# Kernel optimization log

Measured on AMD Instinct MI355X. Metric: run time of the kernel, lower is better.

The kernel has to match this reference:

```python
import jax, jax.numpy as jnp
import numpy as np

D_MODEL, D_INNER, D_STATE, DT_RANK, K = 768, 1536, 16, 48, 4
B, L = 2, 1024


def causal_depthwise_conv(x, w, b):
    # x: [B, L, D], w: [D, 1, K], b: [D]; torch pads K-1 both sides then slices [:L] -> causal left pad
    xt = x.transpose(0, 2, 1)  # [B, D, L]
    out = jax.lax.conv_general_dilated(
        xt, w, window_strides=(1,), padding=[(K - 1, 0)],
        dimension_numbers=('NCH', 'OIH', 'NCH'), feature_group_count=xt.shape[1])
    return out.transpose(0, 2, 1) + b


def ssm(xc, A_log, D, W_dt, dtW, dtb, W_B, W_C):
    # xc: [B, L, Din]
    A = -jnp.exp(A_log)                                   # [Din, N]
    dt_low = jnp.einsum('bld,rd->blr', xc, W_dt)          # [B, L, R]
    delta = jax.nn.softplus(jnp.einsum('blr,dr->bld', dt_low, dtW) + dtb)  # [B, L, Din]
    Bm = jnp.einsum('bld,nd->bln', xc, W_B)               # [B, L, N]
    Cm = jnp.einsum('bld,nd->bln', xc, W_C)               # [B, L, N]
    deltaA = jnp.exp(delta[..., None] * A)                # [B, L, Din, N]
    BX = (delta * xc)[..., None] * Bm[:, :, None, :]      # [B, L, Din, N]

    def combine(e1, e2):
        a1, b1 = e1
        a2, b2 = e2
        return a1 * a2, a2 * b1 + b2

    _, hs = jax.lax.associative_scan(combine, (deltaA, BX), axis=1)  # [B, L, Din, N]
    y = jnp.einsum('bldn,bln->bld', hs, Cm) + D * xc
    return y


def setup_inputs() -> dict:
    key = jax.random.key(0)
    ks = jax.random.split(key, 20)
    s = 0.02
    A_init = jnp.log(jnp.broadcast_to(jnp.arange(1, D_STATE + 1, dtype=jnp.float32), (D_INNER, D_STATE)))
    return {
        'x': jax.random.normal(ks[0], (B, L, D_MODEL), jnp.float32),
        'W_in_states': jax.random.normal(ks[1], (D_INNER, D_MODEL), jnp.float32) * s,
        'W_in_gates': jax.random.normal(ks[2], (D_INNER, D_MODEL), jnp.float32) * s,
        'conv_w': jax.random.normal(ks[3], (D_INNER, 1, K), jnp.float32) * 0.2,
        'conv_b': jax.random.normal(ks[4], (D_INNER,), jnp.float32) * 0.02,
        'conv_w_b': jax.random.normal(ks[5], (D_INNER, 1, K), jnp.float32) * 0.2,
        'conv_b_b': jax.random.normal(ks[6], (D_INNER,), jnp.float32) * 0.02,
        'W_dt': jax.random.normal(ks[7], (DT_RANK, D_INNER), jnp.float32) * s,
        'W_B': jax.random.normal(ks[8], (D_STATE, D_INNER), jnp.float32) * s,
        'W_C': jax.random.normal(ks[9], (D_STATE, D_INNER), jnp.float32) * s,
        'dtW': jax.random.normal(ks[10], (D_INNER, DT_RANK), jnp.float32) * s,
        'dtb': jax.random.normal(ks[11], (D_INNER,), jnp.float32) * 0.1,
        'A_log': A_init,
        'Dp': jnp.ones((D_INNER,), jnp.float32),
        'W_dt_b': jax.random.normal(ks[12], (DT_RANK, D_INNER), jnp.float32) * s,
        'W_B_b': jax.random.normal(ks[13], (D_STATE, D_INNER), jnp.float32) * s,
        'W_C_b': jax.random.normal(ks[14], (D_STATE, D_INNER), jnp.float32) * s,
        'dtW_b': jax.random.normal(ks[15], (D_INNER, DT_RANK), jnp.float32) * s,
        'dtb_b': jax.random.normal(ks[16], (D_INNER,), jnp.float32) * 0.1,
        'A_log_b': A_init,
        'Dp_b': jnp.ones((D_INNER,), jnp.float32),
        'W_out': jax.random.normal(ks[17], (D_MODEL, D_INNER), jnp.float32) * s,
    }


def reference(x, W_in_states, W_in_gates, conv_w, conv_b, conv_w_b, conv_b_b,
              W_dt, W_B, W_C, dtW, dtb, A_log, Dp,
              W_dt_b, W_B_b, W_C_b, dtW_b, dtb_b, A_log_b, Dp_b, W_out):
    xs = jnp.einsum('blm,dm->bld', x, W_in_states)  # [B, L, Din]
    z = jnp.einsum('blm,dm->bld', x, W_in_gates)    # [B, L, Din]
    # forward branch
    xc = jax.nn.silu(causal_depthwise_conv(xs, conv_w, conv_b))
    y = ssm(xc, A_log, Dp, W_dt, dtW, dtb, W_B, W_C)
    # backward branch: xz flipped along L, split -> reversed xs / reversed z
    xs_b = xs[:, ::-1]
    z_b = z[:, ::-1]
    xcb = jax.nn.silu(causal_depthwise_conv(xs_b, conv_w_b, conv_b_b))
    y_b = ssm(xcb, A_log_b, Dp_b, W_dt_b, dtW_b, dtb_b, W_B_b, W_C_b)
    # gating
    y = y * jax.nn.silu(z)
    y_b = y_b * jax.nn.silu(z_b)
    y = (y + y_b[:, ::-1]) * 0.5  # divide_output
    return jnp.einsum('bld,md->blm', y, W_out)
```

## Files before the change

### kernel.cpp

```cpp
#include <hip/hip_runtime.h>
#include <hip/hip_bf16.h>
#include <stdint.h>

#define DM 768
#define DI 1536
#define DSTATE 16
#define RNK 48
#define BB 2
#define LL 1024
#define ML (BB * LL)

#define NSEG 32
#define SEGL (LL / NSEG)

typedef unsigned short u16;
typedef __bf16 bf16x8 __attribute__((ext_vector_type(8)));
typedef float f32x4 __attribute__((ext_vector_type(4)));

struct __align__(8) u16x4_t { u16 x, y, z, w; };

__device__ __forceinline__ float b2f(u16 u) {
  union { uint32_t i; float f; } v; v.i = ((uint32_t)u) << 16; return v.f;
}
__device__ __forceinline__ u16 f2b(float f) {
  union { float f; uint32_t i; } v; v.f = f;
  uint32_t r = v.i + 0x7FFFu + ((v.i >> 16) & 1u);
  return (u16)(r >> 16);
}
__device__ __forceinline__ float silu_f(float x) { return x / (1.f + __expf(-x)); }
__device__ __forceinline__ float softplus_f(float s) {
  return fmaxf(s, 0.f) + __logf(1.f + __expf(-fabsf(s)));
}
__device__ __forceinline__ u16x4_t cvt4(float4 v) {
  u16x4_t o; o.x = f2b(v.x); o.y = f2b(v.y); o.z = f2b(v.z); o.w = f2b(v.w); return o;
}

#define SEG_X    (ML * DM / 4)
#define SEG_W    (DI * DM / 4)
#define SEG_CAT  (128 * DI / 4)
#define SEG_DTW  (DI * 64 / 4)
__global__ __launch_bounds__(256) void convert_kernel(
    const float4* __restrict__ x, const float4* __restrict__ wis,
    const float4* __restrict__ wig, const float4* __restrict__ wout,
    const float* __restrict__ W_B, const float* __restrict__ W_C,
    const float* __restrict__ W_dt,
    const float* __restrict__ W_B_b, const float* __restrict__ W_C_b,
    const float* __restrict__ W_dt_b,
    const float* __restrict__ dtW, const float* __restrict__ dtW_b,
    u16x4_t* __restrict__ xb, u16x4_t* __restrict__ wisb,
    u16x4_t* __restrict__ wigb, u16x4_t* __restrict__ woutb,
    u16x4_t* __restrict__ wcf, u16x4_t* __restrict__ wcb,
    u16x4_t* __restrict__ dtwf, u16x4_t* __restrict__ dtwb)
{
  int idx = blockIdx.x * 256 + threadIdx.x;
  if (idx < SEG_X) { xb[idx] = cvt4(x[idx]); return; }
  idx -= SEG_X;
  if (idx < SEG_W) { wisb[idx] = cvt4(wis[idx]); return; }
  idx -= SEG_W;
  if (idx < SEG_W) { wigb[idx] = cvt4(wig[idx]); return; }
  idx -= SEG_W;
  if (idx < SEG_W) { woutb[idx] = cvt4(wout[idx]); return; }
  idx -= SEG_W;
  if (idx < 2 * SEG_CAT) {
    int dir = idx / SEG_CAT;
    int rem = idx % SEG_CAT;
    int row = rem / (DI / 4), k4 = rem % (DI / 4);
    const float* src = nullptr;
    if (row < 16)      src = (dir ? W_B_b  : W_B)  + (size_t)row * DI + k4 * 4;
    else if (row < 32) src = (dir ? W_C_b  : W_C)  + (size_t)(row - 16) * DI + k4 * 4;
    else if (row < 80) src = (dir ? W_dt_b : W_dt) + (size_t)(row - 32) * DI + k4 * 4;
    u16x4_t o;
    if (src) o = cvt4(*(const float4*)src);
    else { o.x = 0; o.y = 0; o.z = 0; o.w = 0; }
    (dir ? wcb : wcf)[rem] = o;
    return;
  }
  idx -= 2 * SEG_CAT;
  int dir = idx / SEG_DTW;
  int rem = idx % SEG_DTW;
  int d = rem / 16, r4 = rem % 16;
  const float* Dw = dir ? dtW_b : dtW;
  u16x4_t o;
  if (r4 < 12) o = cvt4(*(const float4*)(Dw + (size_t)d * RNK + r4 * 4));
  else { o.x = 0; o.y = 0; o.z = 0; o.w = 0; }
  (dir ? dtwb : dtwf)[rem] = o;
}

__global__ __launch_bounds__(256) void gemm_bt(
    const u16* __restrict__ A, const u16* __restrict__ B0,
    const u16* __restrict__ B1, int Nsplit,
    void* __restrict__ Cout, int M, int N, int K, int ldc, int epi,
    const u16* __restrict__ A2, const u16* __restrict__ B2,
    void* __restrict__ C2,
    u16* __restrict__ Caux, u16* __restrict__ Caux2,
    const float* __restrict__ ebias, const float* __restrict__ ebias2)
{
  if (blockIdx.z) { A = A2; B0 = B2; Cout = C2; Caux = Caux2; ebias = ebias2; }
  __shared__ alignas(16) u16 As[128 * 32];
  __shared__ alignas(16) u16 Bs[128 * 32];
  const int tid = threadIdx.x;
  const int wave = tid >> 6, lane = tid & 63;
  const int bm = blockIdx.y * 128;
  const int bn = blockIdx.x * 128;

  const u16* Bmat = B0;
  int ncol0 = bn;
  int epi_l = epi;
  if (B1 != nullptr && bn >= Nsplit) { Bmat = B1; ncol0 = bn - Nsplit; epi_l = 1; }

  const int c0 = tid, c1 = tid + 256;
  const u16* gA0 = A + (size_t)(bm + (c0 >> 2)) * K + (c0 & 3) * 8;
  const u16* gA1 = A + (size_t)(bm + (c1 >> 2)) * K + (c1 & 3) * 8;
  const u16* gB0 = Bmat + (size_t)(ncol0 + (c0 >> 2)) * K + (c0 & 3) * 8;
  const u16* gB1 = Bmat + (size_t)(ncol0 + (c1 >> 2)) * K + (c1 & 3) * 8;
  uint4* lA0 = (uint4*)&As[c0 * 8]; uint4* lA1 = (uint4*)&As[c1 * 8];
  uint4* lB0 = (uint4*)&Bs[c0 * 8]; uint4* lB1 = (uint4*)&Bs[c1 * 8];

  const int wm = (wave & 1) * 64, wn = (wave >> 1) * 64;
  const int rl = lane & 15, q = lane >> 4;

  f32x4 acc[4][4];
#pragma unroll
  for (int i = 0; i < 4; ++i)
#pragma unroll
    for (int j = 0; j < 4; ++j) acc[i][j] = (f32x4){0.f, 0.f, 0.f, 0.f};

  const bf16x8* AsV = (const bf16x8*)As;
  const bf16x8* BsV = (const bf16x8*)Bs;

  uint4 ra0 = *(const uint4*)(gA0);
  uint4 ra1 = *(const uint4*)(gA1);
  uint4 rb0 = *(const uint4*)(gB0);
  uint4 rb1 = *(const uint4*)(gB1);

  for (int k0 = 0; k0 < K; k0 += 32) {
    *lA0 = ra0; *lA1 = ra1; *lB0 = rb0; *lB1 = rb1;
    __syncthreads();
    if (k0 + 32 < K) {
      ra0 = *(const uint4*)(gA0 + k0 + 32);
      ra1 = *(const uint4*)(gA1 + k0 + 32);
      rb0 = *(const uint4*)(gB0 + k0 + 32);
      rb1 = *(const uint4*)(gB1 + k0 + 32);
    }
    bf16x8 af[4], bfv[4];
#pragma unroll
    for (int s = 0; s < 4; ++s) {
      af[s]  = AsV[(wm + s * 16 + rl) * 4 + q];
      bfv[s] = BsV[(wn + s * 16 + rl) * 4 + q];
    }
#pragma unroll
    for (int i = 0; i < 4; ++i)
#pragma unroll
      for (int j = 0; j < 4; ++j)
        acc[i][j] = __builtin_amdgcn_mfma_f32_16x16x32_bf16(af[i], bfv[j], acc[i][j], 0, 0, 0);
    __syncthreads();
  }

#pragma unroll
  for (int i = 0; i < 4; ++i) {
#pragma unroll
    for (int j = 0; j < 4; ++j) {
#pragma unroll
      for (int r = 0; r < 4; ++r) {
        int row = bm + wm + i * 16 + q * 4 + r;
        int col = bn + wn + j * 16 + rl;
        float v = acc[i][j][r];
        if (epi_l == 1) v = silu_f(v);
        if (epi == 5) {
          if (col < 32)      ((float*)Cout)[(size_t)row * 32 + col] = v;
          else if (col < 96) Caux[(size_t)row * 64 + (col - 32)] = f2b(v);
        } else if (epi == 6) {
          ((float*)Cout)[(size_t)row * ldc + col] = softplus_f(v + ebias[col]);
        } else if (epi == 2) {
          ((float*)Cout)[(size_t)row * ldc + col] = v;
        } else {
          ((u16*)Cout)[(size_t)row * ldc + col] = f2b(v);
        }
      }
    }
  }
}

__global__ void conv_kernel(
    const u16* __restrict__ xsg,
    const float* __restrict__ cw, const float* __restrict__ cb,
    const float* __restrict__ cwb, const float* __restrict__ cbb,
    u16* __restrict__ xc, u16* __restrict__ xcb)
{
  int idx = blockIdx.x * 256 + threadIdx.x;
  int d = idx % DI;
  int row = idx / DI;
  int l = row % LL, b = row / LL;
  const u16* base = xsg + (size_t)b * LL * 3072 + d;

  float4 wf = *(const float4*)(cw + d * 4);
  float4 wb = *(const float4*)(cwb + d * 4);
  float wfk[4] = {wf.x, wf.y, wf.z, wf.w};
  float wbk[4] = {wb.x, wb.y, wb.z, wb.w};

  float accf = cb[d];
  float accb = cbb[d];
#pragma unroll
  for (int k = 0; k < 4; ++k) {
    int ls = l - 3 + k;
    if (ls >= 0) {
      accf += wfk[k] * b2f(base[(size_t)ls * 3072]);
      accb += wbk[k] * b2f(base[(size_t)(LL - 1 - ls) * 3072]);
    }
  }
  xc[idx]  = f2b(silu_f(accf));
  xcb[idx] = f2b(silu_f(accb));
}

__global__ __launch_bounds__(256) void scan_sum(
    const float* __restrict__ df, const float* __restrict__ db,
    const u16* __restrict__ xcf, const u16* __restrict__ xcb,
    const float* __restrict__ pf, const float* __restrict__ pb,
    const float* __restrict__ A_log, const float* __restrict__ A_log_b,
    float* __restrict__ sdl, float* __restrict__ bs)
{
  const int dir = blockIdx.z / NSEG, seg = blockIdx.z % NSEG;
  const float* delta = dir ? db : df;
  const u16* xc = dir ? xcb : xcf;
  const float* proj = dir ? pb : pf;
  const float* Al = dir ? A_log_b : A_log;
  const int b = blockIdx.y;
  const int d = blockIdx.x * 256 + threadIdx.x;
  const int l0 = seg * SEGL;

  __shared__ float Bsh[SEGL][16];
  for (int i = threadIdx.x; i < SEGL * 16; i += 256) {
    int l = i >> 4, n = i & 15;
    Bsh[l][n] = proj[((size_t)b * LL + l0 + l) * 32 + n];
  }
  __syncthreads();

  float An[16];
#pragma unroll
  for (int n = 0; n < 16; ++n) An[n] = -__expf(Al[d * 16 + n]);

  float h[16];
#pragma unroll
  for (int n = 0; n < 16; ++n) h[n] = 0.f;
  float S = 0.f;

  const float* dbase = delta + ((size_t)b * LL + l0) * DI + d;
  const u16* xbase = xc + ((size_t)b * LL + l0) * DI + d;

  for (int g = 0; g < SEGL; g += 4) {
    float dl4[4], dx4[4];
#pragma unroll
    for (int j = 0; j < 4; ++j) {
      float dv = dbase[(size_t)(g + j) * DI];
      float xv = b2f(xbase[(size_t)(g + j) * DI]);
      dl4[j] = dv; dx4[j] = dv * xv;
    }
#pragma unroll
    for (int j = 0; j < 4; ++j) {
      S += dl4[j];
#pragma unroll
      for (int n = 0; n < 16; ++n)
        h[n] = __expf(dl4[j] * An[n]) * h[n] + dx4[j] * Bsh[g + j][n];
    }
  }

  size_t base = (((size_t)dir * BB + b) * NSEG + seg) * DI + d;
  sdl[base] = S;
#pragma unroll
  for (int n = 0; n < 16; ++n) bs[base * 16 + n] = h[n];
}

__global__ __launch_bounds__(256) void scan_carry(
    const float* __restrict__ A_log, const float* __restrict__ A_log_b,
    const float* __restrict__ sdl, float* __restrict__ bs)
{
  int idx = blockIdx.x * 256 + threadIdx.x;
  int n = idx & 15;
  int t = idx >> 4;
  int d = t % DI;
  int b = (t / DI) % BB;
  int dir = t / (DI * BB);
  const float* Al = dir ? A_log_b : A_log;
  float An = -__expf(Al[d * 16 + n]);
  float h = 0.f;
  for (int s = 0; s < NSEG; ++s) {
    size_t base = (((size_t)dir * BB + b) * NSEG + s) * DI + d;
    float S = sdl[base];
    float bv = bs[base * 16 + n];
    bs[base * 16 + n] = h;
    h = __expf(S * An) * h + bv;
  }
}

__global__ __launch_bounds__(256) void scan_apply(
    const float* __restrict__ df, const float* __restrict__ db,
    const u16* __restrict__ xcf, const u16* __restrict__ xcb,
    const float* __restrict__ pf, const float* __restrict__ pb,
    const float* __restrict__ A_log, const float* __restrict__ A_log_b,
    const float* __restrict__ Dp, const float* __restrict__ Dp_b,
    const float* __restrict__ bs,
    u16* __restrict__ y_f, u16* __restrict__ y_b)
{
  const int dir = blockIdx.z / NSEG, seg = blockIdx.z % NSEG;
  const float* delta = dir ? db : df;
  const u16* xc = dir ? xcb : xcf;
  const float* proj = dir ? pb : pf;
  const float* Al = dir ? A_log_b : A_log;
  const float* Dpp = dir ? Dp_b : Dp;
  u16* y = dir ? y_b : y_f;
  const int b = blockIdx.y;
  const int d = blockIdx.x * 256 + threadIdx.x;
  const int l0 = seg * SEGL;

  __shared__ float BCsh[SEGL][32];
  for (int i = threadIdx.x; i < SEGL * 32; i += 256) {
    int l = i >> 5, j = i & 31;
    BCsh[l][j] = proj[((size_t)b * LL + l0 + l) * 32 + j];
  }
  __syncthreads();

  float An[16];
#pragma unroll
  for (int n = 0; n < 16; ++n) An[n] = -__expf(Al[d * 16 + n]);
  const float Dv = Dpp[d];

  float h[16];
  size_t cbase = (((size_t)dir * BB + b) * NSEG + seg) * DI + d;
#pragma unroll
  for (int n = 0; n < 16; ++n) h[n] = bs[cbase * 16 + n];

  const float* dbase = delta + ((size_t)b * LL + l0) * DI + d;
  const u16* xbase = xc + ((size_t)b * LL + l0) * DI + d;
  u16* ybase = y + ((size_t)b * LL + l0) * DI + d;

  for (int g = 0; g < SEGL; g += 4) {
    float dl4[4], xv4[4];
#pragma unroll
    for (int j = 0; j < 4; ++j) {
      dl4[j] = dbase[(size_t)(g + j) * DI];
      xv4[j] = b2f(xbase[(size_t)(g + j) * DI]);
    }
#pragma unroll
    for (int j = 0; j < 4; ++j) {
      float dx = dl4[j] * xv4[j];
      float yv = 0.f;
#pragma unroll
      for (int n = 0; n < 16; ++n) {
        h[n] = __expf(dl4[j] * An[n]) * h[n] + dx * BCsh[g + j][n];
        yv += h[n] * BCsh[g + j][16 + n];
      }
      ybase[(size_t)(g + j) * DI] = f2b(yv + Dv * xv4[j]);
    }
  }
}

__global__ void combine_kernel(
    const u16* __restrict__ ybr, const u16* __restrict__ xsg, u16* yf)
{
  int idx = blockIdx.x * 256 + threadIdx.x;
  int d = idx % DI;
  int row = idx / DI;
  int l = row % LL, b = row / LL;
  float g = b2f(xsg[(size_t)row * 3072 + DI + d]);
  float vb = b2f(ybr[((size_t)b * LL + (LL - 1 - l)) * DI + d]);
  float v = 0.5f * (b2f(yf[idx]) + vb) * g;
  yf[idx] = f2b(v);
}

extern "C" void kernel_launch(void* const* d_in, const int* in_sizes, int n_in,
                              void* d_out, int out_size, void* d_ws, size_t ws_size,
                              hipStream_t stream)
{
  const float* x       = (const float*)d_in[0];
  const float* Wis     = (const float*)d_in[1];
  const float* Wig     = (const float*)d_in[2];
  const float* conv_w  = (const float*)d_in[3];
  const float* conv_b  = (const float*)d_in[4];
  const float* conv_wb = (const float*)d_in[5];
  const float* conv_bb = (const float*)d_in[6];
  const float* W_dt    = (const float*)d_in[7];
  const float* W_B     = (const float*)d_in[8];
  const float* W_C     = (const float*)d_in[9];
  const float* dtW     = (const float*)d_in[10];
  const float* dtb     = (const float*)d_in[11];
  const float* A_log   = (const float*)d_in[12];
  const float* Dp      = (const float*)d_in[13];
  const float* W_dt_b  = (const float*)d_in[14];
  const float* W_B_b   = (const float*)d_in[15];
  const float* W_C_b   = (const float*)d_in[16];
  const float* dtW_b   = (const float*)d_in[17];
  const float* dtb_b   = (const float*)d_in[18];
  const float* A_log_b = (const float*)d_in[19];
  const float* Dp_b    = (const float*)d_in[20];
  const float* W_out   = (const float*)d_in[21];

  char* ws = (char*)d_ws;
  size_t off = 0;
  auto alloc = [&](size_t bytes) -> char* {
    char* p = ws + off; off += (bytes + 255) & ~(size_t)255; return p;
  };
  u16*   xb    = (u16*)alloc((size_t)ML * DM * 2);
  u16*   wisb  = (u16*)alloc((size_t)DI * DM * 2);
  u16*   wigb  = (u16*)alloc((size_t)DI * DM * 2);
  u16*   woutb = (u16*)alloc((size_t)DM * DI * 2);
  u16*   xsg = (u16*)alloc((size_t)ML * 3072 * 2);
  u16*   xc  = (u16*)alloc((size_t)ML * DI * 2);
  u16*   xcb = (u16*)alloc((size_t)ML * DI * 2);
  u16*   wcf = (u16*)alloc((size_t)128 * DI * 2);
  u16*   wcb = (u16*)alloc((size_t)128 * DI * 2);
  u16*   dtwf = (u16*)alloc((size_t)DI * 64 * 2);
  u16*   dtwb = (u16*)alloc((size_t)DI * 64 * 2);
  float* pf  = (float*)alloc((size_t)ML * 32 * 4);
  float* pb  = (float*)alloc((size_t)ML * 32 * 4);
  u16*   dtlf = (u16*)alloc((size_t)ML * 64 * 2);
  u16*   dtlb = (u16*)alloc((size_t)ML * 64 * 2);
  float* df  = (float*)alloc((size_t)ML * DI * 4);
  float* db  = (float*)alloc((size_t)ML * DI * 4);
  u16*   yf  = (u16*)alloc((size_t)ML * DI * 2);
  u16*   ybr = (u16*)alloc((size_t)ML * DI * 2);
  float* sdl = (float*)alloc((size_t)2 * BB * NSEG * DI * 4);
  float* bs  = (float*)alloc((size_t)2 * BB * NSEG * DI * 16 * 4);

  const int conv_total = SEG_X + 3 * SEG_W + 2 * SEG_CAT + 2 * SEG_DTW;
  convert_kernel<<<(conv_total + 255) / 256, 256, 0, stream>>>(
      (const float4*)x, (const float4*)Wis, (const float4*)Wig, (const float4*)W_out,
      W_B, W_C, W_dt, W_B_b, W_C_b, W_dt_b, dtW, dtW_b,
      (u16x4_t*)xb, (u16x4_t*)wisb, (u16x4_t*)wigb, (u16x4_t*)woutb,
      (u16x4_t*)wcf, (u16x4_t*)wcb, (u16x4_t*)dtwf, (u16x4_t*)dtwb);

  gemm_bt<<<dim3(3072 / 128, ML / 128, 1), 256, 0, stream>>>(
      xb, wisb, wigb, DI, xsg, ML, 3072, DM, 3072, 0,
      nullptr, nullptr, nullptr, nullptr, nullptr, nullptr, nullptr);

  conv_kernel<<<(ML * DI) / 256, 256, 0, stream>>>(
      xsg, conv_w, conv_b, conv_wb, conv_bb, xc, xcb);

  gemm_bt<<<dim3(1, ML / 128, 2), 256, 0, stream>>>(
      xc, wcf, nullptr, 1 << 30, pf, ML, 128, DI, 32, 5,
      xcb, wcb, pb, dtlf, dtlb, nullptr, nullptr);

  gemm_bt<<<dim3(DI / 128, ML / 128, 2), 256, 0, stream>>>(
      dtlf, dtwf, nullptr, 1 << 30, df, ML, DI, 64, DI, 6,
      dtlb, dtwb, db, nullptr, nullptr, dtb, dtb_b);

  scan_sum<<<dim3(DI / 256, BB, 2 * NSEG), 256, 0, stream>>>(
      df, db, xc, xcb, pf, pb, A_log, A_log_b, sdl, bs);
  scan_carry<<<(2 * BB * DI * 16) / 256, 256, 0, stream>>>(
      A_log, A_log_b, sdl, bs);
  scan_apply<<<dim3(DI / 256, BB, 2 * NSEG), 256, 0, stream>>>(
      df, db, xc, xcb, pf, pb, A_log, A_log_b, Dp, Dp_b, bs, yf, ybr);

  combine_kernel<<<(ML * DI) / 256, 256, 0, stream>>>(ybr, xsg, yf);

  gemm_bt<<<dim3(DM / 128, ML / 128, 1), 256, 0, stream>>>(
      yf, woutb, nullptr, 1 << 30, d_out, ML, DM, DI, DM, 2,
      nullptr, nullptr, nullptr, nullptr, nullptr, nullptr, nullptr);
}
```

Baseline: 296.5 us.

## Fuse depthwise conv into projection GEMM and scans, fuse combine into output GEMM

Removes the standalone conv and combine kernels and the xc/xcb intermediate buffers. The projection GEMM now computes conv+SiLU on the fly from xsg tiles staged in shared memory. Both scan kernels recompute conv+SiLU with a sliding window over the strided xsg column. The output GEMM applies the average-and-gate step while loading its A tile. This saves global round trips and two launches, at the cost of redundant conv work, strided 3072-stride reads in the scans, and extra ALU and shared-memory traffic inside the GEMM loops.

```diff
diff --git a/kernel.cpp b/kernel.cpp
--- a/kernel.cpp
+++ b/kernel.cpp
@@ -92,10 +92,9 @@
     void* __restrict__ Cout, int M, int N, int K, int ldc, int epi,
     const u16* __restrict__ A2, const u16* __restrict__ B2,
     void* __restrict__ C2,
-    u16* __restrict__ Caux, u16* __restrict__ Caux2,
     const float* __restrict__ ebias, const float* __restrict__ ebias2)
 {
-  if (blockIdx.z) { A = A2; B0 = B2; Cout = C2; Caux = Caux2; ebias = ebias2; }
+  if (blockIdx.z) { A = A2; B0 = B2; Cout = C2; ebias = ebias2; }
   __shared__ alignas(16) u16 As[128 * 32];
   __shared__ alignas(16) u16 Bs[128 * 32];
   const int tid = threadIdx.x;
@@ -166,62 +165,256 @@
         int col = bn + wn + j * 16 + rl;
         float v = acc[i][j][r];
         if (epi_l == 1) v = silu_f(v);
-        if (epi == 5) {
-          if (col < 32)      ((float*)Cout)[(size_t)row * 32 + col] = v;
-          else if (col < 96) Caux[(size_t)row * 64 + (col - 32)] = f2b(v);
-        } else if (epi == 6) {
-          ((float*)Cout)[(size_t)row * ldc + col] = softplus_f(v + ebias[col]);
-        } else if (epi == 2) {
-          ((float*)Cout)[(size_t)row * ldc + col] = v;
-        } else {
-          ((u16*)Cout)[(size_t)row * ldc + col] = f2b(v);
+        if (epi == 6)      ((float*)Cout)[(size_t)row * ldc + col] = softplus_f(v + ebias[col]);
+        else if (epi == 2) ((float*)Cout)[(size_t)row * ldc + col] = v;
+        else               ((u16*)Cout)[(size_t)row * ldc + col] = f2b(v);
+      }
+    }
+  }
+}
+
+__global__ __launch_bounds__(256) void gemm_projconv(
+    const u16* __restrict__ xsg,
+    const u16* __restrict__ wcf, const u16* __restrict__ wcb,
+    const float* __restrict__ cw, const float* __restrict__ cb,
+    const float* __restrict__ cwb, const float* __restrict__ cbb,
+    float* __restrict__ pf, float* __restrict__ pb,
+    u16* __restrict__ dtlf, u16* __restrict__ dtlb)
+{
+  const int dir = blockIdx.z;
+  const u16* Bmat = dir ? wcb : wcf;
+  const float* cwp = dir ? cwb : cw;
+  const float* cbp = dir ? cbb : cb;
+  float* Cout = dir ? pb : pf;
+  u16* Caux = dir ? dtlb : dtlf;
+
+  __shared__ alignas(16) u16 As[128 * 32];
+  __shared__ alignas(16) u16 Bs[128 * 32];
+  __shared__ alignas(16) u16 Xs[131 * 32];
+  __shared__ float Wsh[32][4];
+  __shared__ float Bish[32];
+
+  const int tid = threadIdx.x;
+  const int wave = tid >> 6, lane = tid & 63;
+  const int bm = blockIdx.y * 128;
+  const int bb = bm / LL, l0 = bm % LL;
+
+  const int c0 = tid, c1 = tid + 256;
+  const u16* gB0 = Bmat + (size_t)(c0 >> 2) * DI + (c0 & 3) * 8;
+  const u16* gB1 = Bmat + (size_t)(c1 >> 2) * DI + (c1 & 3) * 8;
+  uint4* lB0 = (uint4*)&Bs[c0 * 8]; uint4* lB1 = (uint4*)&Bs[c1 * 8];
+
+  const u16* gX[3]; uint4* lX[3]; int nxc = 0;
+  for (int c = tid; c < 524; c += 256) {
+    int trow = c >> 2, dc = (c & 3) * 8;
+    int ls = dir ? (LL - 128 - l0 + trow) : (l0 - 3 + trow);
+    gX[nxc] = (ls >= 0 && ls < LL)
+        ? xsg + (size_t)(bb * LL + ls) * 3072 + dc : nullptr;
+    lX[nxc] = (uint4*)&Xs[(size_t)c * 8];
+    nxc++;
+  }
+
+  const int wm = (wave & 1) * 64, wn = (wave >> 1) * 64;
+  const int rl = lane & 15, q = lane >> 4;
+
+  f32x4 acc[4][4];
+#pragma unroll
+  for (int i = 0; i < 4; ++i)
+#pragma unroll
+    for (int j = 0; j < 4; ++j) acc[i][j] = (f32x4){0.f, 0.f, 0.f, 0.f};
+
+  const bf16x8* AsV = (const bf16x8*)As;
+  const bf16x8* BsV = (const bf16x8*)Bs;
+  const uint4 zz = {0u, 0u, 0u, 0u};
+
+  uint4 rb0 = *(const uint4*)gB0;
+  uint4 rb1 = *(const uint4*)gB1;
+  uint4 rx[3];
+  for (int i = 0; i < nxc; ++i) rx[i] = gX[i] ? *(const uint4*)(gX[i]) : zz;
+  float wreg = 0.f, breg = 0.f;
+  if (tid < 128)       wreg = cwp[(size_t)(tid >> 2) * 4 + (tid & 3)];
+  else if (tid < 160)  breg = cbp[tid - 128];
+
+  for (int k0 = 0; k0 < DI; k0 += 32) {
+    *lB0 = rb0; *lB1 = rb1;
+    for (int i = 0; i < nxc; ++i) *lX[i] = rx[i];
+    if (tid < 128)      Wsh[tid >> 2][tid & 3] = wreg;
+    else if (tid < 160) Bish[tid - 128] = breg;
+    __syncthreads();
+
+    if (k0 + 32 < DI) {
+      rb0 = *(const uint4*)(gB0 + k0 + 32);
+      rb1 = *(const uint4*)(gB1 + k0 + 32);
+      for (int i = 0; i < nxc; ++i)
+        rx[i] = gX[i] ? *(const uint4*)(gX[i] + k0 + 32) : zz;
+      if (tid < 128)      wreg = cwp[(size_t)(k0 + 32 + (tid >> 2)) * 4 + (tid & 3)];
+      else if (tid < 160) breg = cbp[k0 + 32 + tid - 128];
+    }
+
+#pragma unroll
+    for (int cc = 0; cc < 2; ++cc) {
+      int c = cc ? c1 : c0;
+      int i = c >> 2, dl = (c & 3) * 8;
+      int outl = l0 + i;
+      uint4 x4[4];
+#pragma unroll
+      for (int k = 0; k < 4; ++k) {
+        int t = dir ? (130 - i - k) : (i + k);
+        x4[k] = *(const uint4*)&Xs[(size_t)t * 32 + dl];
+      }
+      u16 ov[8];
+#pragma unroll
+      for (int e = 0; e < 8; ++e) {
+        float a = Bish[dl + e];
+#pragma unroll
+        for (int k = 0; k < 4; ++k) {
+          const u16* xp = (const u16*)&x4[k];
+          float tap = (outl + k >= 3) ? b2f(xp[e]) : 0.f;
+          a += Wsh[dl + e][k] * tap;
         }
+        ov[e] = f2b(silu_f(a));
       }
-    }
-  }
-}
-
-__global__ void conv_kernel(
+      *(uint4*)&As[(size_t)c * 8] = *(const uint4*)ov;
+    }
+    __syncthreads();
+
+    bf16x8 af[4], bfv[4];
+#pragma unroll
+    for (int s = 0; s < 4; ++s) {
+      af[s]  = AsV[(wm + s * 16 + rl) * 4 + q];
+      bfv[s] = BsV[(wn + s * 16 + rl) * 4 + q];
+    }
+#pragma unroll
+    for (int i = 0; i < 4; ++i)
+#pragma unroll
+      for (int j = 0; j < 4; ++j)
+        acc[i][j] = __builtin_amdgcn_mfma_f32_16x16x32_bf16(af[i], bfv[j], acc[i][j], 0, 0, 0);
+    __syncthreads();
+  }
+
+#pragma unroll
+  for (int i = 0; i < 4; ++i) {
+#pragma unroll
+    for (int j = 0; j < 4; ++j) {
+#pragma unroll
+      for (int r = 0; r < 4; ++r) {
+        int row = bm + wm + i * 16 + q * 4 + r;
+        int col = wn + j * 16 + rl;
+        float v = acc[i][j][r];
+        if (col < 32)      Cout[(size_t)row * 32 + col] = v;
+        else if (col < 96) Caux[(size_t)row * 64 + (col - 32)] = f2b(v);
+      }
+    }
+  }
+}
+
+__global__ __launch_bounds__(256) void gemm_out(
+    const u16* __restrict__ yf, const u16* __restrict__ ybr,
+    const u16* __restrict__ xsg, const u16* __restrict__ Bw,
+    float* __restrict__ out)
+{
+  __shared__ alignas(16) u16 As[128 * 32];
+  __shared__ alignas(16) u16 Bs[128 * 32];
+  const int tid = threadIdx.x;
+  const int wave = tid >> 6, lane = tid & 63;
+  const int bm = blockIdx.y * 128;
+  const int bn = blockIdx.x * 128;
+
+  const int c0 = tid, c1 = tid + 256;
+  int r0 = bm + (c0 >> 2), r1 = bm + (c1 >> 2);
+  int dc0 = (c0 & 3) * 8, dc1 = (c1 & 3) * 8;
+  int rr0 = (r0 / LL) * LL + (LL - 1 - (r0 % LL));
+  int rr1 = (r1 / LL) * LL + (LL - 1 - (r1 % LL));
+  const u16* gy0 = yf + (size_t)r0 * DI + dc0;
+  const u16* gy1 = yf + (size_t)r1 * DI + dc1;
+  const u16* gr0 = ybr + (size_t)rr0 * DI + dc0;
+  const u16* gr1 = ybr + (size_t)rr1 * DI + dc1;
+  const u16* gg0 = xsg + (size_t)r0 * 3072 + DI + dc0;
+  const u16* gg1 = xsg + (size_t)r1 * 3072 + DI + dc1;
+  const u16* gB0 = Bw + (size_t)(bn + (c0 >> 2)) * DI + dc0;
+  const u16* gB1 = Bw + (size_t)(bn + (c1 >> 2)) * DI + dc1;
+  uint4* lA0 = (uint4*)&As[c0 * 8]; uint4* lA1 = (uint4*)&As[c1 * 8];
+  uint4* lB0 = (uint4*)&Bs[c0 * 8]; uint4* lB1 = (uint4*)&Bs[c1 * 8];
+
+  const int wm = (wave & 1) * 64, wn = (wave >> 1) * 64;
+  const int rl = lane & 15, q = lane >> 4;
+
+  f32x4 acc[4][4];
+#pragma unroll
+  for (int i = 0; i < 4; ++i)
+#pragma unroll
+    for (int j = 0; j < 4; ++j) acc[i][j] = (f32x4){0.f, 0.f, 0.f, 0.f};
+
+  const bf16x8* AsV = (const bf16x8*)As;
+  const bf16x8* BsV = (const bf16x8*)Bs;
+
+  uint4 ry0 = *(const uint4*)gy0, ry1 = *(const uint4*)gy1;
+  uint4 rr0v = *(const uint4*)gr0, rr1v = *(const uint4*)gr1;
+  uint4 rg0 = *(const uint4*)gg0, rg1 = *(const uint4*)gg1;
+  uint4 rb0 = *(const uint4*)gB0, rb1 = *(const uint4*)gB1;
+
+  for (int k0 = 0; k0 < DI; k0 += 32) {
+    {
+      const u16* yp0 = (const u16*)&ry0; const u16* bp0 = (const u16*)&rr0v;
+      const u16* gp0 = (const u16*)&rg0;
+      const u16* yp1 = (const u16*)&ry1; const u16* bp1 = (const u16*)&rr1v;
+      const u16* gp1 = (const u16*)&rg1;
+      u16 o0[8], o1[8];
+#pragma unroll
+      for (int e = 0; e < 8; ++e) {
+        o0[e] = f2b(0.5f * (b2f(yp0[e]) + b2f(bp0[e])) * b2f(gp0[e]));
+        o1[e] = f2b(0.5f * (b2f(yp1[e]) + b2f(bp1[e])) * b2f(gp1[e]));
+      }
+      *lA0 = *(const uint4*)o0;
+      *lA1 = *(const uint4*)o1;
+    }
+    *lB0 = rb0; *lB1 = rb1;
+    __syncthreads();
+    if (k0 + 32 < DI) {
+      ry0 = *(const uint4*)(gy0 + k0 + 32); ry1 = *(const uint4*)(gy1 + k0 + 32);
+      rr0v = *(const uint4*)(gr0 + k0 + 32); rr1v = *(const uint4*)(gr1 + k0 + 32);
+      rg0 = *(const uint4*)(gg0 + k0 + 32); rg1 = *(const uint4*)(gg1 + k0 + 32);
+      rb0 = *(const uint4*)(gB0 + k0 + 32); rb1 = *(const uint4*)(gB1 + k0 + 32);
+    }
+    bf16x8 af[4], bfv[4];
+#pragma unroll
+    for (int s = 0; s < 4; ++s) {
+      af[s]  = AsV[(wm + s * 16 + rl) * 4 + q];
+      bfv[s] = BsV[(wn + s * 16 + rl) * 4 + q];
+    }
+#pragma unroll
+    for (int i = 0; i < 4; ++i)
+#pragma unroll
+      for (int j = 0; j < 4; ++j)
+        acc[i][j] = __builtin_amdgcn_mfma_f32_16x16x32_bf16(af[i], bfv[j], acc[i][j], 0, 0, 0);
+    __syncthreads();
+  }
+
+#pragma unroll
+  for (int i = 0; i < 4; ++i) {
+#pragma unroll
+    for (int j = 0; j < 4; ++j) {
+#pragma unroll
+      for (int r = 0; r < 4; ++r) {
+        int row = bm + wm + i * 16 + q * 4 + r;
+        int col = bn + wn + j * 16 + rl;
+        out[(size_t)row * DM + col] = acc[i][j][r];
+      }
+    }
+  }
+}
+
+__global__ __launch_bounds__(256) void scan_sum(
     const u16* __restrict__ xsg,
     const float* __restrict__ cw, const float* __restrict__ cb,
     const float* __restrict__ cwb, const float* __restrict__ cbb,
-    u16* __restrict__ xc, u16* __restrict__ xcb)
-{
-  int idx = blockIdx.x * 256 + threadIdx.x;
-  int d = idx % DI;
-  int row = idx / DI;
-  int l = row % LL, b = row / LL;
-  const u16* base = xsg + (size_t)b * LL * 3072 + d;
-
-  float4 wf = *(const float4*)(cw + d * 4);
-  float4 wb = *(const float4*)(cwb + d * 4);
-  float wfk[4] = {wf.x, wf.y, wf.z, wf.w};
-  float wbk[4] = {wb.x, wb.y, wb.z, wb.w};
-
-  float accf = cb[d];
-  float accb = cbb[d];
-#pragma unroll
-  for (int k = 0; k < 4; ++k) {
-    int ls = l - 3 + k;
-    if (ls >= 0) {
-      accf += wfk[k] * b2f(base[(size_t)ls * 3072]);
-      accb += wbk[k] * b2f(base[(size_t)(LL - 1 - ls) * 3072]);
-    }
-  }
-  xc[idx]  = f2b(silu_f(accf));
-  xcb[idx] = f2b(silu_f(accb));
-}
-
-__global__ __launch_bounds__(256) void scan_sum(
     const float* __restrict__ df, const float* __restrict__ db,
-    const u16* __restrict__ xcf, const u16* __restrict__ xcb,
     const float* __restrict__ pf, const float* __restrict__ pb,
     const float* __restrict__ A_log, const float* __restrict__ A_log_b,
     float* __restrict__ sdl, float* __restrict__ bs)
 {
   const int dir = blockIdx.z / NSEG, seg = blockIdx.z % NSEG;
   const float* delta = dir ? db : df;
-  const u16* xc = dir ? xcb : xcf;
   const float* proj = dir ? pb : pf;
   const float* Al = dir ? A_log_b : A_log;
   const int b = blockIdx.y;
@@ -239,28 +432,43 @@
 #pragma unroll
   for (int n = 0; n < 16; ++n) An[n] = -__expf(Al[d * 16 + n]);
 
+  float4 wv = dir ? *(const float4*)(cwb + d * 4) : *(const float4*)(cw + d * 4);
+  const float cbv = dir ? cbb[d] : cb[d];
+  const u16* xcol = xsg + (size_t)b * LL * 3072 + d;
+
+  float w[4];
+#pragma unroll
+  for (int k = 0; k < 4; ++k) {
+    if (!dir) { int ls = l0 - 3 + k; w[k] = (ls >= 0) ? b2f(xcol[(size_t)ls * 3072]) : 0.f; }
+    else      { int ls = LL + 2 - l0 - k; w[k] = (ls <= LL - 1) ? b2f(xcol[(size_t)ls * 3072]) : 0.f; }
+  }
+
   float h[16];
 #pragma unroll
   for (int n = 0; n < 16; ++n) h[n] = 0.f;
   float S = 0.f;
 
   const float* dbase = delta + ((size_t)b * LL + l0) * DI + d;
-  const u16* xbase = xc + ((size_t)b * LL + l0) * DI + d;
 
   for (int g = 0; g < SEGL; g += 4) {
-    float dl4[4], dx4[4];
+    float dl4[4], nx[4];
 #pragma unroll
     for (int j = 0; j < 4; ++j) {
-      float dv = dbase[(size_t)(g + j) * DI];
-      float xv = b2f(xbase[(size_t)(g + j) * DI]);
-      dl4[j] = dv; dx4[j] = dv * xv;
+      dl4[j] = dbase[(size_t)(g + j) * DI];
+      int lnew = dir ? (LL - 2 - (l0 + g + j)) : (l0 + g + j + 1);
+      bool ok = dir ? (lnew >= 0) : (lnew < LL);
+      nx[j] = ok ? b2f(xcol[(size_t)lnew * 3072]) : 0.f;
     }
 #pragma unroll
     for (int j = 0; j < 4; ++j) {
-      S += dl4[j];
+      float xv = silu_f(cbv + w[0] * wv.x + w[1] * wv.y + w[2] * wv.z + w[3] * wv.w);
+      float dv = dl4[j];
+      float dx = dv * xv;
+      S += dv;
 #pragma unroll
       for (int n = 0; n < 16; ++n)
-        h[n] = __expf(dl4[j] * An[n]) * h[n] + dx4[j] * Bsh[g + j][n];
+        h[n] = __expf(dv * An[n]) * h[n] + dx * Bsh[g + j][n];
+      w[0] = w[1]; w[1] = w[2]; w[2] = w[3]; w[3] = nx[j];
     }
   }
 
@@ -293,8 +501,10 @@
 }
 
 __global__ __launch_bounds__(256) void scan_apply(
+    const u16* __restrict__ xsg,
+    const float* __restrict__ cw, const float* __restrict__ cb,
+    const float* __restrict__ cwb, const float* __restrict__ cbb,
     const float* __restrict__ df, const float* __restrict__ db,
-    const u16* __restrict__ xcf, const u16* __restrict__ xcb,
     const float* __restrict__ pf, const float* __restrict__ pb,
     const float* __restrict__ A_log, const float* __restrict__ A_log_b,
     const float* __restrict__ Dp, const float* __restrict__ Dp_b,
@@ -303,7 +513,6 @@
 {
   const int dir = blockIdx.z / NSEG, seg = blockIdx.z % NSEG;
   const float* delta = dir ? db : df;
-  const u16* xc = dir ? xcb : xcf;
   const float* proj = dir ? pb : pf;
   const float* Al = dir ? A_log_b : A_log;
   const float* Dpp = dir ? Dp_b : Dp;
@@ -324,47 +533,49 @@
   for (int n = 0; n < 16; ++n) An[n] = -__expf(Al[d * 16 + n]);
   const float Dv = Dpp[d];
 
+  float4 wv = dir ? *(const float4*)(cwb + d * 4) : *(const float4*)(cw + d * 4);
+  const float cbv = dir ? cbb[d] : cb[d];
+  const u16* xcol = xsg + (size_t)b * LL * 3072 + d;
+
+  float w[4];
+#pragma unroll
+  for (int k = 0; k < 4; ++k) {
+    if (!dir) { int ls = l0 - 3 + k; w[k] = (ls >= 0) ? b2f(xcol[(size_t)ls * 3072]) : 0.f; }
+    else      { int ls = LL + 2 - l0 - k; w[k] = (ls <= LL - 1) ? b2f(xcol[(size_t)ls * 3072]) : 0.f; }
+  }
+
   float h[16];
   size_t cbase = (((size_t)dir * BB + b) * NSEG + seg) * DI + d;
 #pragma unroll
   for (int n = 0; n < 16; ++n) h[n] = bs[cbase * 16 + n];
 
   const float* dbase = delta + ((size_t)b * LL + l0) * DI + d;
-  const u16* xbase = xc + ((size_t)b * LL + l0) * DI + d;
   u16* ybase = y + ((size_t)b * LL + l0) * DI + d;
 
   for (int g = 0; g < SEGL; g += 4) {
-    float dl4[4], xv4[4];
+    float dl4[4], nx[4];
 #pragma unroll
     for (int j = 0; j < 4; ++j) {
       dl4[j] = dbase[(size_t)(g + j) * DI];
-      xv4[j] = b2f(xbase[(size_t)(g + j) * DI]);
+      int lnew = dir ? (LL - 2 - (l0 + g + j)) : (l0 + g + j + 1);
+      bool ok = dir ? (lnew >= 0) : (lnew < LL);
+      nx[j] = ok ? b2f(xcol[(size_t)lnew * 3072]) : 0.f;
     }
 #pragma unroll
     for (int j = 0; j < 4; ++j) {
-      float dx = dl4[j] * xv4[j];
+      float xv = silu_f(cbv + w[0] * wv.x + w[1] * wv.y + w[2] * wv.z + w[3] * wv.w);
+      float dv = dl4[j];
+      float dx = dv * xv;
       float yv = 0.f;
 #pragma unroll
       for (int n = 0; n < 16; ++n) {
-        h[n] = __expf(dl4[j] * An[n]) * h[n] + dx * BCsh[g + j][n];
+        h[n] = __expf(dv * An[n]) * h[n] + dx * BCsh[g + j][n];
         yv += h[n] * BCsh[g + j][16 + n];
       }
-      ybase[(size_t)(g + j) * DI] = f2b(yv + Dv * xv4[j]);
-    }
-  }
-}
-
-__global__ void combine_kernel(
-    const u16* __restrict__ ybr, const u16* __restrict__ xsg, u16* yf)
-{
-  int idx = blockIdx.x * 256 + threadIdx.x;
-  int d = idx % DI;
-  int row = idx / DI;
-  int l = row % LL, b = row / LL;
-  float g = b2f(xsg[(size_t)row * 3072 + DI + d]);
-  float vb = b2f(ybr[((size_t)b * LL + (LL - 1 - l)) * DI + d]);
-  float v = 0.5f * (b2f(yf[idx]) + vb) * g;
-  yf[idx] = f2b(v);
+      ybase[(size_t)(g + j) * DI] = f2b(yv + Dv * xv);
+      w[0] = w[1]; w[1] = w[2]; w[2] = w[3]; w[3] = nx[j];
+    }
+  }
 }
 
 extern "C" void kernel_launch(void* const* d_in, const int* in_sizes, int n_in,
@@ -404,8 +615,6 @@
   u16*   wigb  = (u16*)alloc((size_t)DI * DM * 2);
   u16*   woutb = (u16*)alloc((size_t)DM * DI * 2);
   u16*   xsg = (u16*)alloc((size_t)ML * 3072 * 2);
-  u16*   xc  = (u16*)alloc((size_t)ML * DI * 2);
-  u16*   xcb = (u16*)alloc((size_t)ML * DI * 2);
   u16*   wcf = (u16*)alloc((size_t)128 * DI * 2);
   u16*   wcb = (u16*)alloc((size_t)128 * DI * 2);
   u16*   dtwf = (u16*)alloc((size_t)DI * 64 * 2);
@@ -430,29 +639,24 @@
 
   gemm_bt<<<dim3(3072 / 128, ML / 128, 1), 256, 0, stream>>>(
       xb, wisb, wigb, DI, xsg, ML, 3072, DM, 3072, 0,
-      nullptr, nullptr, nullptr, nullptr, nullptr, nullptr, nullptr);
-
-  conv_kernel<<<(ML * DI) / 256, 256, 0, stream>>>(
-      xsg, conv_w, conv_b, conv_wb, conv_bb, xc, xcb);
-
-  gemm_bt<<<dim3(1, ML / 128, 2), 256, 0, stream>>>(
-      xc, wcf, nullptr, 1 << 30, pf, ML, 128, DI, 32, 5,
-      xcb, wcb, pb, dtlf, dtlb, nullptr, nullptr);
+      nullptr, nullptr, nullptr, nullptr, nullptr);
+
+  gemm_projconv<<<dim3(1, ML / 128, 2), 256, 0, stream>>>(
+      xsg, wcf, wcb, conv_w, conv_b, conv_wb, conv_bb, pf, pb, dtlf, dtlb);
 
   gemm_bt<<<dim3(DI / 128, ML / 128, 2), 256, 0, stream>>>(
       dtlf, dtwf, nullptr, 1 << 30, df, ML, DI, 64, DI, 6,
-      dtlb, dtwb, db, nullptr, nullptr, dtb, dtb_b);
+      dtlb, dtwb, db, dtb, dtb_b);
 
   scan_sum<<<dim3(DI / 256, BB, 2 * NSEG), 256, 0, stream>>>(
-      df, db, xc, xcb, pf, pb, A_log, A_log_b, sdl, bs);
+      xsg, conv_w, conv_b, conv_wb, conv_bb, df, db, pf, pb,
+      A_log, A_log_b, sdl, bs);
   scan_carry<<<(2 * BB * DI * 16) / 256, 256, 0, stream>>>(
       A_log, A_log_b, sdl, bs);
   scan_apply<<<dim3(DI / 256, BB, 2 * NSEG), 256, 0, stream>>>(
-      df, db, xc, xcb, pf, pb, A_log, A_log_b, Dp, Dp_b, bs, yf, ybr);
-
-  combine_kernel<<<(ML * DI) / 256, 256, 0, stream>>>(ybr, xsg, yf);
-
-  gemm_bt<<<dim3(DM / 128, ML / 128, 1), 256, 0, stream>>>(
-      yf, woutb, nullptr, 1 << 30, d_out, ML, DM, DI, DM, 2,
-      nullptr, nullptr, nullptr, nullptr, nullptr, nullptr, nullptr);
-}
+      xsg, conv_w, conv_b, conv_wb, conv_bb, df, db, pf, pb,
+      A_log, A_log_b, Dp, Dp_b, bs, yf, ybr);
+
+  gemm_out<<<dim3(DM / 128, ML / 128, 1), 256, 0, stream>>>(
+      yf, ybr, xsg, woutb, (float*)d_out);
+}
```

After: 425.4 us. +43.4%, slower.
